# Kernel optimization log

Hardware: AMD Instinct MI355X
Metric: run time of the kernel (lower is better)

Reference implementation:

```python
import jax, jax.numpy as jnp
import numpy as np

T, B, OBS, H, A = 512, 64, 512, 1024, 18


def setup_inputs() -> dict:
    key = jax.random.key(0)
    ks = jax.random.split(key, 8)
    s = lambda fan: 1.0 / np.sqrt(fan)
    return {
        "obs": jax.random.normal(ks[0], (T, B, OBS), jnp.float32),
        # binary done/valid mask per (timestep, env)
        "mask": (jax.random.uniform(ks[1], (T, B)) > 0.05).astype(jnp.float32),
        "W_enc": jax.random.normal(ks[2], (H, OBS), jnp.float32) * s(OBS),
        "b_enc": jnp.zeros((H,), jnp.float32),
        "W_ih": jax.random.normal(ks[3], (4 * H, H), jnp.float32) * s(H),
        "b_ih": jnp.zeros((4 * H,), jnp.float32),
        "W_hh": jax.random.normal(ks[4], (4 * H, H), jnp.float32) * s(H),
        "b_hh": jnp.zeros((4 * H,), jnp.float32),
        "W_dec": jax.random.normal(ks[5], (A, H), jnp.float32) * s(H),
        "b_dec": jnp.zeros((A,), jnp.float32),
    }


def reference(obs, mask, W_enc, b_enc, W_ih, b_ih, W_hh, b_hh, W_dec, b_dec):
    # encoder MLP + relu, batched over all T*B (one big GEMM)
    encoded = jax.nn.relu(jnp.einsum("tbo,ho->tbh", obs, W_enc) + b_enc)
    # precompute input contribution to LSTM gates for all timesteps: [T,B,4H]
    x_gates = jnp.einsum("tbh,gh->tbg", encoded, W_ih) + b_ih + b_hh

    def step(carry, inp):
        h, c = carry
        xg, m = inp  # xg: [B,4H], m: [B]
        gates = xg + h @ W_hh.T
        i, f, g, o = jnp.split(gates, 4, axis=-1)  # torch LSTMCell order
        c_new = jax.nn.sigmoid(f) * c + jax.nn.sigmoid(i) * jnp.tanh(g)
        h_new = jax.nn.sigmoid(o) * jnp.tanh(c_new)
        m = m[:, None]
        h_new = h_new * m
        c_new = c_new * m
        return (h_new, c_new), h_new

    h0 = jnp.zeros((B, H), jnp.float32)
    c0 = jnp.zeros((B, H), jnp.float32)
    (h, c), latent = jax.lax.scan(step, (h0, c0), (x_gates, mask))

    # decoder over flattened (T*B, H) then mask q-values
    values = jnp.einsum("tbh,ah->tba", latent, W_dec) + b_dec
    values = values * mask[..., None]
    return values, h, c
```

## Files before the change

### kernel.cpp

```cpp
#include <hip/hip_runtime.h>
#include <hip/hip_bf16.h>

#define T_ 512
#define B_ 64
#define OBS_ 512
#define H_ 1024
#define A_ 18
#define MM_ (T_*B_)
#define G4_ (4*H_)
#define CH_ 64
#define NCH_ (T_/CH_)
#define CM_ (CH_*B_)

typedef unsigned short u16;
typedef unsigned long long u64;
typedef __attribute__((ext_vector_type(8))) short s8v;
typedef __attribute__((ext_vector_type(4))) float f4v;

__device__ __forceinline__ float b2f(u16 u){
    unsigned x = ((unsigned)u) << 16;
    return __builtin_bit_cast(float, x);
}
__device__ __forceinline__ u16 f2b(float f){
    unsigned x = __builtin_bit_cast(unsigned, f);
    return (u16)((x + 0x7fffu + ((x >> 16) & 1u)) >> 16);
}

__device__ __forceinline__ float fsig(float x){
    return __builtin_amdgcn_rcpf(1.f + __expf(-x));
}
__device__ __forceinline__ float ftanh(float x){
    return 1.f - 2.f * __builtin_amdgcn_rcpf(__expf(2.f * x) + 1.f);
}


__global__ void prep_all(const float* __restrict__ Wenc, const float* __restrict__ Wih,
                         const float* __restrict__ Whh, const float* __restrict__ Wdec,
                         const float* __restrict__ bih, const float* __restrict__ bhh,
                         u16* __restrict__ wenc_b, u16* __restrict__ wih_b,
                         u16* __restrict__ whh_b, u16* __restrict__ wdec_b,
                         float* __restrict__ bias2, u16* __restrict__ h_hist,
                         float* __restrict__ c_f32, unsigned* __restrict__ flags)
{
    int i = blockIdx.x * blockDim.x + threadIdx.x;
    int stride = gridDim.x * blockDim.x;
    for (int k = i; k < G4_ * H_; k += stride){
        wih_b[k] = f2b(Wih[k]);
        whh_b[k] = f2b(Whh[k]);
    }
    for (int k = i; k < H_ * OBS_; k += stride) wenc_b[k] = f2b(Wenc[k]);
    for (int k = i; k < A_ * H_; k += stride) wdec_b[k] = f2b(Wdec[k]);
    for (int k = i; k < G4_; k += stride) bias2[k] = bih[k] + bhh[k];
    unsigned* h0 = (unsigned*)h_hist;
    for (int k = i; k < B_ * H_ / 2; k += stride) h0[k] = 0u;
    for (int k = i; k < B_ * H_; k += stride) c_f32[k] = 0.f;
    for (int k = i; k < 1024; k += stride) flags[k] = 0u;
}

__global__ void copy_hc(const float* __restrict__ h, const float* __restrict__ c,
                        float* __restrict__ out){
    int i = blockIdx.x * blockDim.x + threadIdx.x;
    out[(size_t)MM_*A_ + i] = h[i];
    out[(size_t)MM_*A_ + B_*H_ + i] = c[i];
}


#define LDSS 72

template<bool A_FP32, bool RELU>
__global__ __launch_bounds__(256) void gemm_bt(
    const void* __restrict__ Aptr, const u16* __restrict__ W,
    const float* __restrict__ bias, u16* __restrict__ C,
    int M, int N, int K)
{
    __shared__ __align__(16) u16 As[128 * LDSS];
    __shared__ __align__(16) u16 Bs[128 * LDSS];

    const int tid  = threadIdx.x;
    const int lane = tid & 63;
    const int wid  = tid >> 6;
    const int wm   = wid & 1, wn = wid >> 1;
    const int m0   = blockIdx.y * 128, n0 = blockIdx.x * 128;
    const int quad = lane >> 4, l16 = lane & 15;

    f4v acc[4][4];
    #pragma unroll
    for (int i = 0; i < 4; i++)
        #pragma unroll
        for (int j = 0; j < 4; j++) acc[i][j] = (f4v){0.f,0.f,0.f,0.f};

    for (int k0 = 0; k0 < K; k0 += 64){
        __syncthreads();
        if (A_FP32){
            const float* A = (const float*)Aptr;
            #pragma unroll
            for (int pss = 0; pss < 8; pss++){
                int idx = pss * 256 + tid;
                int row = idx >> 4, ch = idx & 15;
                float4 v = *(const float4*)(A + (size_t)(m0 + row) * K + k0 + ch * 4);
                u16* d = &As[row * LDSS + ch * 4];
                d[0] = f2b(v.x); d[1] = f2b(v.y); d[2] = f2b(v.z); d[3] = f2b(v.w);
            }
        } else {
            const u16* A = (const u16*)Aptr;
            #pragma unroll
            for (int pss = 0; pss < 4; pss++){
                int idx = pss * 256 + tid;
                int row = idx >> 3, ch = idx & 7;
                *(uint4*)&As[row * LDSS + ch * 8] =
                    *(const uint4*)(A + (size_t)(m0 + row) * K + k0 + ch * 8);
            }
        }
        #pragma unroll
        for (int pss = 0; pss < 4; pss++){
            int idx = pss * 256 + tid;
            int row = idx >> 3, ch = idx & 7;
            *(uint4*)&Bs[row * LDSS + ch * 8] =
                *(const uint4*)(W + (size_t)(n0 + row) * K + k0 + ch * 8);
        }
        __syncthreads();

        #pragma unroll
        for (int kk = 0; kk < 64; kk += 32){
            s8v af[4], bf[4];
            #pragma unroll
            for (int mt = 0; mt < 4; mt++)
                af[mt] = *(const s8v*)&As[(wm*64 + mt*16 + l16) * LDSS + kk + quad*8];
            #pragma unroll
            for (int nt = 0; nt < 4; nt++)
                bf[nt] = *(const s8v*)&Bs[(wn*64 + nt*16 + l16) * LDSS + kk + quad*8];
            #pragma unroll
            for (int mt = 0; mt < 4; mt++)
                #pragma unroll
                for (int nt = 0; nt < 4; nt++)
                    acc[mt][nt] = __builtin_amdgcn_mfma_f32_16x16x32_bf16(
                        af[mt], bf[nt], acc[mt][nt], 0, 0, 0);
        }
    }

    #pragma unroll
    for (int mt = 0; mt < 4; mt++){
        #pragma unroll
        for (int nt = 0; nt < 4; nt++){
            #pragma unroll
            for (int r = 0; r < 4; r++){
                int m = m0 + wm*64 + mt*16 + quad*4 + r;
                int n = n0 + wn*64 + nt*16 + l16;
                float v = acc[mt][nt][r] + bias[n];
                if (RELU) v = fmaxf(v, 0.f);
                C[(size_t)m * N + n] = f2b(v);
            }
        }
    }
}


__global__ __launch_bounds__(256, 1) void lstm_scan(
    const u16* __restrict__ xg,
    const u16* __restrict__ Whh,
    u16* __restrict__ h_hist,
    float* __restrict__ c_glob,
    float* __restrict__ h_f32,
    const float* __restrict__ mask,
    unsigned* __restrict__ flags,
    int t0)
{
    __shared__ float red[4][4][16][17];

    const int tid  = threadIdx.x;
    const int lane = tid & 63;
    const int w    = tid >> 6;
    const int quad = lane >> 4, l16 = lane & 15;
    const int bid  = blockIdx.x;
    const int g = bid & 3, s = bid >> 2;
    const int rb0 = g * 16, j0 = s * 16;

    const int koff = w * 256;
    s8v bf[4][8];
    #pragma unroll
    for (int gate = 0; gate < 4; gate++)
        #pragma unroll
        for (int ks = 0; ks < 8; ks++)
            bf[gate][ks] = *(const s8v*)(
                Whh + (size_t)(gate * H_ + j0 + l16) * H_ + koff + ks * 32 + quad * 8);

    const int cb = tid >> 4, cu = tid & 15;
    const size_t cidx = (size_t)(rb0 + cb) * H_ + j0 + cu;
    float c_reg = c_glob[cidx];

    const size_t hoff = (size_t)(rb0 + l16) * H_ + koff + quad * 8;

    unsigned* myflag = flags + (g << 8) + (s << 2) + w;
    const unsigned* pollp = flags + (g << 8) + (w << 6) + lane;

    const u16* xg0 = xg + (size_t)(rb0 + cb) * G4_ + j0 + cu;
    u16 nxi = xg0[0], nxf = xg0[H_], nxv = xg0[2 * H_], nxo = xg0[3 * H_];
    float nm = mask[rb0 + cb];

    for (int st = 0; st < CH_; st++){
        const float xi = b2f(nxi), xf = b2f(nxf), xv = b2f(nxv), xo = b2f(nxo);
        const float m = nm;

        const unsigned tgt = (unsigned)(t0 + st);
        int tries = 0;
        for (;;){
            unsigned f = __hip_atomic_load(pollp, __ATOMIC_RELAXED, __HIP_MEMORY_SCOPE_AGENT);
            if (__all((int)(f >= tgt))) break;
            if (++tries > (1 << 20)) break;
            if (tries >= 8) __builtin_amdgcn_s_sleep(1);
        }

        const u16* hs = h_hist + (size_t)st * B_ * H_ + hoff;
        f4v acc[4];
        #pragma unroll
        for (int gate = 0; gate < 4; gate++) acc[gate] = (f4v){0.f,0.f,0.f,0.f};
        #pragma unroll
        for (int ks = 0; ks < 8; ks++){
            s8v af = *(const s8v*)(hs + ks * 32);
            #pragma unroll
            for (int gate = 0; gate < 4; gate++)
                acc[gate] = __builtin_amdgcn_mfma_f32_16x16x32_bf16(af, bf[gate][ks], acc[gate], 0, 0, 0);
        }
        #pragma unroll
        for (int gate = 0; gate < 4; gate++)
            #pragma unroll
            for (int r = 0; r < 4; r++)
                red[w][gate][quad * 4 + r][l16] = acc[gate][r];
        __syncthreads();

        float gi = xi, gf = xf, gg = xv, go = xo;
        #pragma unroll
        for (int ww = 0; ww < 4; ww++){
            gi += red[ww][0][cb][cu];
            gf += red[ww][1][cb][cu];
            gg += red[ww][2][cb][cu];
            go += red[ww][3][cb][cu];
        }

        float is = fsig(gi);
        float fs = fsig(gf);
        float os = fsig(go);
        float gt = ftanh(gg);

        float cn = fs * c_reg + is * gt;
        float hn = os * ftanh(cn);
        hn *= m; cn *= m;
        c_reg = cn;
        if (t0 + st == T_ - 1) h_f32[cidx] = hn;

        unsigned hb = (unsigned)f2b(hn);
        unsigned partner = (unsigned)__shfl_xor((int)hb, 1, 64);
        if ((cu & 1) == 0){
            unsigned packed = hb | (partner << 16);
            unsigned* dst = (unsigned*)(h_hist + (size_t)(st + 1) * B_ * H_ + cidx);
            __hip_atomic_store(dst, packed, __ATOMIC_RELAXED, __HIP_MEMORY_SCOPE_AGENT);
            if (st == CH_ - 1){
                unsigned* dst0 = (unsigned*)(h_hist + cidx);
                __hip_atomic_store(dst0, packed, __ATOMIC_RELAXED, __HIP_MEMORY_SCOPE_AGENT);
            }
        }
        asm volatile("s_waitcnt vmcnt(0)" ::: "memory");

        if (lane == 0)
            __hip_atomic_store(myflag, (unsigned)(t0 + st + 1),
                               __ATOMIC_RELAXED, __HIP_MEMORY_SCOPE_AGENT);

        if (st + 1 < CH_){
            const u16* xgn = xg + (size_t)(st + 1) * B_ * G4_ + (size_t)(rb0 + cb) * G4_ + j0 + cu;
            nxi = xgn[0]; nxf = xgn[H_]; nxv = xgn[2 * H_]; nxo = xgn[3 * H_];
            nm = mask[(size_t)(st + 1) * B_ + rb0 + cb];
        }

        __syncthreads();
    }

    c_glob[cidx] = c_reg;
}


__global__ __launch_bounds__(256) void decode_kernel(
    const u16* __restrict__ latent, const u16* __restrict__ Wdec,
    const float* __restrict__ bdec, const float* __restrict__ mask,
    float* __restrict__ values, int rows)
{
    __shared__ __align__(16) u16 wl[A_ * H_];
    const int tid = threadIdx.x;
    for (int i = tid; i < A_ * H_ / 8; i += 256)
        ((uint4*)wl)[i] = ((const uint4*)Wdec)[i];
    __syncthreads();

    const int lane = tid & 63;
    int wid = blockIdx.x * 4 + (tid >> 6);
    const int nwaves = gridDim.x * 4;

    for (int row = wid; row < rows; row += nwaves){
        float lat[16];
        #pragma unroll
        for (int i = 0; i < 16; i++)
            lat[i] = b2f(latent[(size_t)row * H_ + i*64 + lane]);
        float acc[A_];
        #pragma unroll
        for (int a = 0; a < A_; a++) acc[a] = 0.f;
        #pragma unroll
        for (int i = 0; i < 16; i++){
            #pragma unroll
            for (int a = 0; a < A_; a++)
                acc[a] += lat[i] * b2f(wl[a * H_ + i*64 + lane]);
        }
        float m = mask[row];
        #pragma unroll
        for (int a = 0; a < A_; a++){
            float v = acc[a];
            #pragma unroll
            for (int s = 32; s > 0; s >>= 1) v += __shfl_down(v, s, 64);
            if (lane == 0) values[(size_t)row * A_ + a] = (v + bdec[a]) * m;
        }
    }
}


extern "C" void kernel_launch(void* const* d_in, const int* in_sizes, int n_in,
                              void* d_out, int out_size, void* d_ws, size_t ws_size,
                              hipStream_t stream)
{
    const float* obs  = (const float*)d_in[0];
    const float* mask = (const float*)d_in[1];
    const float* Wenc = (const float*)d_in[2];
    const float* benc = (const float*)d_in[3];
    const float* Wih  = (const float*)d_in[4];
    const float* bih  = (const float*)d_in[5];
    const float* Whh  = (const float*)d_in[6];
    const float* bhh  = (const float*)d_in[7];
    const float* Wdec = (const float*)d_in[8];
    const float* bdec = (const float*)d_in[9];
    float* out = (float*)d_out;

    char* p = (char*)d_ws;
    size_t o = 0;
    auto alloc = [&](size_t bytes){ void* r = p + o; o += (bytes + 255) & ~(size_t)255; return r; };
    u16*      wenc_b  = (u16*)     alloc((size_t)H_ * OBS_ * 2);
    u16*      wih_b   = (u16*)     alloc((size_t)G4_ * H_ * 2);
    u16*      whh_b   = (u16*)     alloc((size_t)G4_ * H_ * 2);
    u16*      wdec_b  = (u16*)     alloc((size_t)A_ * H_ * 2);
    float*    bias2   = (float*)   alloc((size_t)G4_ * 4);
    u16*      h_hist  = (u16*)     alloc((size_t)(CH_ + 1) * B_ * H_ * 2);
    float*    h_f32   = (float*)   alloc((size_t)B_ * H_ * 4);
    float*    c_f32   = (float*)   alloc((size_t)B_ * H_ * 4);
    unsigned* flags   = (unsigned*)alloc(1024 * 4);
    u16*      xg_ch   = (u16*)     alloc((size_t)CM_ * G4_ * 2);

    const size_t enc_all_b = (size_t)MM_ * H_ * 2;
    const bool big = ws_size >= o + enc_all_b + 4096;
    (void)in_sizes; (void)n_in; (void)out_size;

    prep_all<<<2048, 256, 0, stream>>>(Wenc, Wih, Whh, Wdec, bih, bhh,
                                       wenc_b, wih_b, whh_b, wdec_b,
                                       bias2, h_hist, c_f32, flags);

    if (big){
        u16* enc_all = (u16*)alloc(enc_all_b);

        dim3 ge(H_ / 128, MM_ / 128);
        gemm_bt<true, true><<<ge, 256, 0, stream>>>(
            obs, wenc_b, benc, enc_all, MM_, H_, OBS_);

        for (int c = 0; c < NCH_; c++){
            const int t0 = c * CH_;

            dim3 gx(G4_ / 128, CM_ / 128);
            gemm_bt<false, false><<<gx, 256, 0, stream>>>(
                enc_all + (size_t)c * CM_ * H_, wih_b, bias2, xg_ch, CM_, G4_, H_);

            lstm_scan<<<256, 256, 0, stream>>>(
                xg_ch, whh_b, h_hist, c_f32, h_f32,
                mask + (size_t)t0 * B_, flags, t0);

            decode_kernel<<<256, 256, 0, stream>>>(
                h_hist + (size_t)B_ * H_, wdec_b, bdec, mask + (size_t)t0 * B_,
                out + (size_t)t0 * B_ * A_, CM_);
        }
    } else {
        u16* enc_ch = (u16*)alloc((size_t)CM_ * H_ * 2);

        for (int c = 0; c < NCH_; c++){
            const int t0 = c * CH_;

            dim3 g1(H_ / 128, CM_ / 128);
            gemm_bt<true, true><<<g1, 256, 0, stream>>>(
                obs + (size_t)t0 * B_ * OBS_, wenc_b, benc, enc_ch, CM_, H_, OBS_);

            dim3 g2(G4_ / 128, CM_ / 128);
            gemm_bt<false, false><<<g2, 256, 0, stream>>>(
                enc_ch, wih_b, bias2, xg_ch, CM_, G4_, H_);

            lstm_scan<<<256, 256, 0, stream>>>(
                xg_ch, whh_b, h_hist, c_f32, h_f32,
                mask + (size_t)t0 * B_, flags, t0);

            decode_kernel<<<256, 256, 0, stream>>>(
                h_hist + (size_t)B_ * H_, wdec_b, bdec, mask + (size_t)t0 * B_,
                out + (size_t)t0 * B_ * A_, CM_);
        }
    }

    copy_hc<<<256, 256, 0, stream>>>(h_f32, c_f32, out);
}
```

Baseline: 2.575 ms.

## Fuse input-gate projection into persistent LSTM scan and run all timesteps in one launch

Drops the separate x_gates GEMM. Each scan block keeps its slice of W_ih in registers next to W_hh and computes the input-gate contribution with MFMA before it waits on the step flag, so that work can overlap the inter-block synchronisation. In the big-workspace path, the scan covers all 512 steps in one launch over a full h history buffer, and a single decode runs afterwards. This removes per-chunk launches and the xg round trip through memory. In exchange it doubles per-thread register pressure for weights and puts extra MFMA work on the serial critical path of each step.

Result: no change. 2.555 ms (-0.8%).

```diff
diff --git a/kernel.cpp b/kernel.cpp
--- a/kernel.cpp
+++ b/kernel.cpp
@@ -39,7 +39,7 @@
                          const float* __restrict__ bih, const float* __restrict__ bhh,
                          u16* __restrict__ wenc_b, u16* __restrict__ wih_b,
                          u16* __restrict__ whh_b, u16* __restrict__ wdec_b,
-                         float* __restrict__ bias2, u16* __restrict__ h_hist,
+                         float* __restrict__ bias2, u16* __restrict__ h0buf,
                          float* __restrict__ c_f32, unsigned* __restrict__ flags)
 {
     int i = blockIdx.x * blockDim.x + threadIdx.x;
@@ -51,7 +51,7 @@
     for (int k = i; k < H_ * OBS_; k += stride) wenc_b[k] = f2b(Wenc[k]);
     for (int k = i; k < A_ * H_; k += stride) wdec_b[k] = f2b(Wdec[k]);
     for (int k = i; k < G4_; k += stride) bias2[k] = bih[k] + bhh[k];
-    unsigned* h0 = (unsigned*)h_hist;
+    unsigned* h0 = (unsigned*)h0buf;
     for (int k = i; k < B_ * H_ / 2; k += stride) h0[k] = 0u;
     for (int k = i; k < B_ * H_; k += stride) c_f32[k] = 0.f;
     for (int k = i; k < 1024; k += stride) flags[k] = 0u;
@@ -67,9 +67,8 @@
 
 #define LDSS 72
 
-template<bool A_FP32, bool RELU>
-__global__ __launch_bounds__(256) void gemm_bt(
-    const void* __restrict__ Aptr, const u16* __restrict__ W,
+__global__ __launch_bounds__(256) void gemm_enc(
+    const float* __restrict__ A, const u16* __restrict__ W,
     const float* __restrict__ bias, u16* __restrict__ C,
     int M, int N, int K)
 {
@@ -91,25 +90,13 @@
 
     for (int k0 = 0; k0 < K; k0 += 64){
         __syncthreads();
-        if (A_FP32){
-            const float* A = (const float*)Aptr;
-            #pragma unroll
-            for (int pss = 0; pss < 8; pss++){
-                int idx = pss * 256 + tid;
-                int row = idx >> 4, ch = idx & 15;
-                float4 v = *(const float4*)(A + (size_t)(m0 + row) * K + k0 + ch * 4);
-                u16* d = &As[row * LDSS + ch * 4];
-                d[0] = f2b(v.x); d[1] = f2b(v.y); d[2] = f2b(v.z); d[3] = f2b(v.w);
-            }
-        } else {
-            const u16* A = (const u16*)Aptr;
-            #pragma unroll
-            for (int pss = 0; pss < 4; pss++){
-                int idx = pss * 256 + tid;
-                int row = idx >> 3, ch = idx & 7;
-                *(uint4*)&As[row * LDSS + ch * 8] =
-                    *(const uint4*)(A + (size_t)(m0 + row) * K + k0 + ch * 8);
-            }
+        #pragma unroll
+        for (int pss = 0; pss < 8; pss++){
+            int idx = pss * 256 + tid;
+            int row = idx >> 4, ch = idx & 15;
+            float4 v = *(const float4*)(A + (size_t)(m0 + row) * K + k0 + ch * 4);
+            u16* d = &As[row * LDSS + ch * 4];
+            d[0] = f2b(v.x); d[1] = f2b(v.y); d[2] = f2b(v.z); d[3] = f2b(v.w);
         }
         #pragma unroll
         for (int pss = 0; pss < 4; pss++){
@@ -146,9 +133,7 @@
             for (int r = 0; r < 4; r++){
                 int m = m0 + wm*64 + mt*16 + quad*4 + r;
                 int n = n0 + wn*64 + nt*16 + l16;
-                float v = acc[mt][nt][r] + bias[n];
-                if (RELU) v = fmaxf(v, 0.f);
-                C[(size_t)m * N + n] = f2b(v);
+                C[(size_t)m * N + n] = f2b(fmaxf(acc[mt][nt][r] + bias[n], 0.f));
             }
         }
     }
@@ -156,14 +141,16 @@
 
 
 __global__ __launch_bounds__(256, 1) void lstm_scan(
-    const u16* __restrict__ xg,
+    const u16* __restrict__ enc,
+    const u16* __restrict__ Wih,
     const u16* __restrict__ Whh,
+    const float* __restrict__ bias2,
     u16* __restrict__ h_hist,
     float* __restrict__ c_glob,
     float* __restrict__ h_f32,
     const float* __restrict__ mask,
     unsigned* __restrict__ flags,
-    int t0)
+    int t0, int nsteps, u16* __restrict__ seed)
 {
     __shared__ float red[4][4][16][17];
 
@@ -176,30 +163,49 @@
     const int rb0 = g * 16, j0 = s * 16;
 
     const int koff = w * 256;
-    s8v bf[4][8];
+    s8v bf[4][8], wf[4][8];
     #pragma unroll
     for (int gate = 0; gate < 4; gate++)
         #pragma unroll
-        for (int ks = 0; ks < 8; ks++)
-            bf[gate][ks] = *(const s8v*)(
-                Whh + (size_t)(gate * H_ + j0 + l16) * H_ + koff + ks * 32 + quad * 8);
+        for (int ks = 0; ks < 8; ks++){
+            size_t off = (size_t)(gate * H_ + j0 + l16) * H_ + koff + ks * 32 + quad * 8;
+            bf[gate][ks] = *(const s8v*)(Whh + off);
+            wf[gate][ks] = *(const s8v*)(Wih + off);
+        }
 
     const int cb = tid >> 4, cu = tid & 15;
     const size_t cidx = (size_t)(rb0 + cb) * H_ + j0 + cu;
     float c_reg = c_glob[cidx];
 
+    float br[4];
+    #pragma unroll
+    for (int gate = 0; gate < 4; gate++) br[gate] = bias2[gate * H_ + j0 + cu];
+
     const size_t hoff = (size_t)(rb0 + l16) * H_ + koff + quad * 8;
+    const size_t eoff = (size_t)(rb0 + l16) * H_ + koff + quad * 8;
 
     unsigned* myflag = flags + (g << 8) + (s << 2) + w;
     const unsigned* pollp = flags + (g << 8) + (w << 6) + lane;
 
-    const u16* xg0 = xg + (size_t)(rb0 + cb) * G4_ + j0 + cu;
-    u16 nxi = xg0[0], nxf = xg0[H_], nxv = xg0[2 * H_], nxo = xg0[3 * H_];
+    s8v ef[8];
+    {
+        const u16* es = enc + eoff;
+        #pragma unroll
+        for (int ks = 0; ks < 8; ks++) ef[ks] = *(const s8v*)(es + ks * 32);
+    }
     float nm = mask[rb0 + cb];
 
-    for (int st = 0; st < CH_; st++){
-        const float xi = b2f(nxi), xf = b2f(nxf), xv = b2f(nxv), xo = b2f(nxo);
+    for (int st = 0; st < nsteps; st++){
         const float m = nm;
+
+        f4v acc[4];
+        #pragma unroll
+        for (int gate = 0; gate < 4; gate++) acc[gate] = (f4v){0.f,0.f,0.f,0.f};
+        #pragma unroll
+        for (int ks = 0; ks < 8; ks++)
+            #pragma unroll
+            for (int gate = 0; gate < 4; gate++)
+                acc[gate] = __builtin_amdgcn_mfma_f32_16x16x32_bf16(ef[ks], wf[gate][ks], acc[gate], 0, 0, 0);
 
         const unsigned tgt = (unsigned)(t0 + st);
         int tries = 0;
@@ -211,9 +217,6 @@
         }
 
         const u16* hs = h_hist + (size_t)st * B_ * H_ + hoff;
-        f4v acc[4];
-        #pragma unroll
-        for (int gate = 0; gate < 4; gate++) acc[gate] = (f4v){0.f,0.f,0.f,0.f};
         #pragma unroll
         for (int ks = 0; ks < 8; ks++){
             s8v af = *(const s8v*)(hs + ks * 32);
@@ -228,7 +231,7 @@
                 red[w][gate][quad * 4 + r][l16] = acc[gate][r];
         __syncthreads();
 
-        float gi = xi, gf = xf, gg = xv, go = xo;
+        float gi = br[0], gf = br[1], gg = br[2], go = br[3];
         #pragma unroll
         for (int ww = 0; ww < 4; ww++){
             gi += red[ww][0][cb][cu];
@@ -254,8 +257,8 @@
             unsigned packed = hb | (partner << 16);
             unsigned* dst = (unsigned*)(h_hist + (size_t)(st + 1) * B_ * H_ + cidx);
             __hip_atomic_store(dst, packed, __ATOMIC_RELAXED, __HIP_MEMORY_SCOPE_AGENT);
-            if (st == CH_ - 1){
-                unsigned* dst0 = (unsigned*)(h_hist + cidx);
+            if (seed && st == nsteps - 1){
+                unsigned* dst0 = (unsigned*)(seed + cidx);
                 __hip_atomic_store(dst0, packed, __ATOMIC_RELAXED, __HIP_MEMORY_SCOPE_AGENT);
             }
         }
@@ -265,9 +268,10 @@
             __hip_atomic_store(myflag, (unsigned)(t0 + st + 1),
                                __ATOMIC_RELAXED, __HIP_MEMORY_SCOPE_AGENT);
 
-        if (st + 1 < CH_){
-            const u16* xgn = xg + (size_t)(st + 1) * B_ * G4_ + (size_t)(rb0 + cb) * G4_ + j0 + cu;
-            nxi = xgn[0]; nxf = xgn[H_]; nxv = xgn[2 * H_]; nxo = xgn[3 * H_];
+        if (st + 1 < nsteps){
+            const u16* es = enc + (size_t)(st + 1) * B_ * H_ + eoff;
+            #pragma unroll
+            for (int ks = 0; ks < 8; ks++) ef[ks] = *(const s8v*)(es + ks * 32);
             nm = mask[(size_t)(st + 1) * B_ + rb0 + cb];
         }
 
@@ -343,64 +347,55 @@
     u16*      whh_b   = (u16*)     alloc((size_t)G4_ * H_ * 2);
     u16*      wdec_b  = (u16*)     alloc((size_t)A_ * H_ * 2);
     float*    bias2   = (float*)   alloc((size_t)G4_ * 4);
-    u16*      h_hist  = (u16*)     alloc((size_t)(CH_ + 1) * B_ * H_ * 2);
     float*    h_f32   = (float*)   alloc((size_t)B_ * H_ * 4);
     float*    c_f32   = (float*)   alloc((size_t)B_ * H_ * 4);
     unsigned* flags   = (unsigned*)alloc(1024 * 4);
-    u16*      xg_ch   = (u16*)     alloc((size_t)CM_ * G4_ * 2);
-
+
+    const size_t hall_b    = (size_t)(T_ + 1) * B_ * H_ * 2;
     const size_t enc_all_b = (size_t)MM_ * H_ * 2;
-    const bool big = ws_size >= o + enc_all_b + 4096;
+    const bool big = ws_size >= o + hall_b + enc_all_b + 65536;
     (void)in_sizes; (void)n_in; (void)out_size;
 
-    prep_all<<<2048, 256, 0, stream>>>(Wenc, Wih, Whh, Wdec, bih, bhh,
-                                       wenc_b, wih_b, whh_b, wdec_b,
-                                       bias2, h_hist, c_f32, flags);
-
     if (big){
+        u16* h_all   = (u16*)alloc(hall_b);
         u16* enc_all = (u16*)alloc(enc_all_b);
 
+        prep_all<<<2048, 256, 0, stream>>>(Wenc, Wih, Whh, Wdec, bih, bhh,
+                                           wenc_b, wih_b, whh_b, wdec_b,
+                                           bias2, h_all, c_f32, flags);
+
         dim3 ge(H_ / 128, MM_ / 128);
-        gemm_bt<true, true><<<ge, 256, 0, stream>>>(
-            obs, wenc_b, benc, enc_all, MM_, H_, OBS_);
+        gemm_enc<<<ge, 256, 0, stream>>>(obs, wenc_b, benc, enc_all, MM_, H_, OBS_);
+
+        lstm_scan<<<256, 256, 0, stream>>>(
+            enc_all, wih_b, whh_b, bias2, h_all, c_f32, h_f32,
+            mask, flags, 0, T_, nullptr);
+
+        decode_kernel<<<2048, 256, 0, stream>>>(
+            h_all + (size_t)B_ * H_, wdec_b, bdec, mask, out, MM_);
+    } else {
+        u16* h_hist = (u16*)alloc((size_t)(CH_ + 1) * B_ * H_ * 2);
+        u16* enc_ch = (u16*)alloc((size_t)CM_ * H_ * 2);
+
+        prep_all<<<2048, 256, 0, stream>>>(Wenc, Wih, Whh, Wdec, bih, bhh,
+                                           wenc_b, wih_b, whh_b, wdec_b,
+                                           bias2, h_hist, c_f32, flags);
 
         for (int c = 0; c < NCH_; c++){
             const int t0 = c * CH_;
 
-            dim3 gx(G4_ / 128, CM_ / 128);
-            gemm_bt<false, false><<<gx, 256, 0, stream>>>(
-                enc_all + (size_t)c * CM_ * H_, wih_b, bias2, xg_ch, CM_, G4_, H_);
+            dim3 g1(H_ / 128, CM_ / 128);
+            gemm_enc<<<g1, 256, 0, stream>>>(
+                obs + (size_t)t0 * B_ * OBS_, wenc_b, benc, enc_ch, CM_, H_, OBS_);
 
             lstm_scan<<<256, 256, 0, stream>>>(
-                xg_ch, whh_b, h_hist, c_f32, h_f32,
-                mask + (size_t)t0 * B_, flags, t0);
+                enc_ch, wih_b, whh_b, bias2, h_hist, c_f32, h_f32,
+                mask + (size_t)t0 * B_, flags, t0, CH_, h_hist);
 
             decode_kernel<<<256, 256, 0, stream>>>(
                 h_hist + (size_t)B_ * H_, wdec_b, bdec, mask + (size_t)t0 * B_,
                 out + (size_t)t0 * B_ * A_, CM_);
         }
-    } else {
-        u16* enc_ch = (u16*)alloc((size_t)CM_ * H_ * 2);
-
-        for (int c = 0; c < NCH_; c++){
-            const int t0 = c * CH_;
-
-            dim3 g1(H_ / 128, CM_ / 128);
-            gemm_bt<true, true><<<g1, 256, 0, stream>>>(
-                obs + (size_t)t0 * B_ * OBS_, wenc_b, benc, enc_ch, CM_, H_, OBS_);
-
-            dim3 g2(G4_ / 128, CM_ / 128);
-            gemm_bt<false, false><<<g2, 256, 0, stream>>>(
-                enc_ch, wih_b, bias2, xg_ch, CM_, G4_, H_);
-
-            lstm_scan<<<256, 256, 0, stream>>>(
-                xg_ch, whh_b, h_hist, c_f32, h_f32,
-                mask + (size_t)t0 * B_, flags, t0);
-
-            decode_kernel<<<256, 256, 0, stream>>>(
-                h_hist + (size_t)B_ * H_, wdec_b, bdec, mask + (size_t)t0 * B_,
-                out + (size_t)t0 * B_ * A_, CM_);
-        }
     }
 
     copy_hc<<<256, 256, 0, stream>>>(h_f32, c_f32, out);
```
